# Performance work log

Hardware: AMD Instinct MI355X
Metric: run time of the kernel (lower is better)

Reference implementation:

```python
import jax, jax.numpy as jnp
import numpy as np

B, S, D_IN, H, L = 8, 4096, 256, 512, 2
EPS = 1e-5


def layer_norm(x, w, b):
    mu = x.mean(axis=-1, keepdims=True)
    var = ((x - mu) ** 2).mean(axis=-1, keepdims=True)
    return (x - mu) * jax.lax.rsqrt(var + EPS) * w + b


def rwkv_scan(k, v):
    # wkv_t = sigmoid(k_t)*v_t + alpha_{t-1};  alpha_t = sigmoid(k_t)*v_t + 0.9*alpha_{t-1}
    s = jax.nn.sigmoid(k) * v  # [B,S,H]
    def step(alpha, s_t):
        wkv_t = s_t + alpha
        return s_t + 0.9 * alpha, wkv_t
    _, wkv = jax.lax.scan(step, jnp.zeros_like(s[:, 0]), jnp.swapaxes(s, 0, 1))
    return jnp.swapaxes(wkv, 0, 1)


def setup_inputs() -> dict:
    key = jax.random.key(0)
    ks = jax.random.split(key, 16)
    sc = 1.0 / np.sqrt(H)
    return {
        "x": jax.random.normal(ks[0], (B, S, D_IN), jnp.float32),
        "W_in": jax.random.normal(ks[1], (H, D_IN), jnp.float32) / np.sqrt(D_IN),
        "b_in": jnp.zeros((H,), jnp.float32),
        "tm_k": jax.random.normal(ks[2], (L, H), jnp.float32),
        "tm_v": jax.random.normal(ks[3], (L, H), jnp.float32),
        "tm_r": jax.random.normal(ks[4], (L, H), jnp.float32),
        "Wk": jax.random.normal(ks[5], (L, H, H), jnp.float32) * sc,
        "Wv": jax.random.normal(ks[6], (L, H, H), jnp.float32) * sc,
        "Wr": jax.random.normal(ks[7], (L, H, H), jnp.float32) * sc,
        "Wo": jax.random.normal(ks[8], (L, H, H), jnp.float32) * sc,
        "ln1_w": jnp.ones((L, H), jnp.float32),
        "ln1_b": jnp.zeros((L, H), jnp.float32),
        "ln2_w": jnp.ones((L, H), jnp.float32),
        "ln2_b": jnp.zeros((L, H), jnp.float32),
    }


def reference(x, W_in, b_in, tm_k, tm_v, tm_r, Wk, Wv, Wr, Wo, ln1_w, ln1_b, ln2_w, ln2_b):
    h = jnp.einsum('bsd,hd->bsh', x, W_in) + b_in  # input projection
    for l in range(L):
        mean = h.mean(axis=1, keepdims=True)  # [B,1,H]
        xk = h * tm_k[l] + (1 - tm_k[l]) * mean
        xv = h * tm_v[l] + (1 - tm_v[l]) * mean
        xr = h * tm_r[l] + (1 - tm_r[l]) * mean
        k = jax.nn.relu(jnp.einsum('bsh,oh->bso', xk, Wk[l]))
        v = jax.nn.relu(jnp.einsum('bsh,oh->bso', xv, Wv[l]))
        r = jax.nn.sigmoid(jnp.einsum('bsh,oh->bso', xr, Wr[l]))
        wkv = rwkv_scan(k, v)
        out = jnp.einsum('bsh,oh->bso', r * wkv, Wo[l])
        out = layer_norm(h + out, ln1_w[l], ln1_b[l])
        ff = jax.nn.relu(layer_norm(out, ln2_w[l], ln2_b[l]))
        h = out + ff
    return h
```

## Files before the change

### kernel.cpp

```cpp
#include <hip/hip_runtime.h>
#include <hip/hip_bf16.h>
#include <cstdint>
#include <cstddef>

#define S_LEN 4096
#define HDIM  512
#define BDIM  8
#define DIN   256
#define NLAYER 2

using float4v = __attribute__((ext_vector_type(4))) float;
using short8  = __attribute__((ext_vector_type(8))) short;
using bf16x8  = __attribute__((ext_vector_type(8))) __bf16;

struct __align__(8) us4_t { unsigned short x, y, z, w; };

__device__ __forceinline__ unsigned short f2bf(float f) {
    return __builtin_bit_cast(unsigned short, (__bf16)f);
}
__device__ __forceinline__ float bf2f(unsigned short s) {
    union { unsigned u; float f; } v; v.u = ((unsigned)s) << 16;
    return v.f;
}
__device__ __forceinline__ float fast_rcp(float x) { return __builtin_amdgcn_rcpf(x); }
__device__ __forceinline__ float fast_rsq(float x) { return __builtin_amdgcn_rsqf(x); }

__device__ __forceinline__ float4v mfma_bf16(short8 a, short8 b, float4v c) {
    return __builtin_amdgcn_mfma_f32_16x16x32_bf16(
        __builtin_bit_cast(bf16x8, a), __builtin_bit_cast(bf16x8, b), c, 0, 0, 0);
}
__device__ __forceinline__ float wave_sum(float v) {
#pragma unroll
    for (int m = 1; m < 64; m <<= 1) v += __shfl_xor(v, m, 64);
    return v;
}
__device__ __forceinline__ void gload16(const void* g, void* l) {
    __builtin_amdgcn_global_load_lds(
        (const __attribute__((address_space(1))) unsigned int*)g,
        (__attribute__((address_space(3))) unsigned int*)l,
        16, 0, 0);
}

#define VMW_ASM(N) asm volatile("s_waitcnt vmcnt(" #N ")" ::: "memory")
template<int N> __device__ __forceinline__ void vmwait() {
    static_assert(N == 0 || N == 4 || N == 6 || N == 8 || N == 10,
                  "add a case for this N");
    if constexpr (N == 0) VMW_ASM(0);
    else if constexpr (N == 4) VMW_ASM(4);
    else if constexpr (N == 6) VMW_ASM(6);
    else if constexpr (N == 8) VMW_ASM(8);
    else if constexpr (N == 10) VMW_ASM(10);
}
#define LGKM0()    asm volatile("s_waitcnt lgkmcnt(0)" ::: "memory")
#define RBARRIER() asm volatile("s_barrier" ::: "memory")

__global__ void cvt_k(const float* __restrict__ in, unsigned short* __restrict__ out, int n4) {
    int i = blockIdx.x * blockDim.x + threadIdx.x;
    if (i >= n4) return;
    float4 v = ((const float4*)in)[i];
    us4_t o;
    o.x = f2bf(v.x); o.y = f2bf(v.y); o.z = f2bf(v.z); o.w = f2bf(v.w);
    ((us4_t*)out)[i] = o;
}

__global__ void cvtw_k(const float* __restrict__ Wk, const float* __restrict__ Wv,
                       const float* __restrict__ Wr,
                       const float* __restrict__ tmk, const float* __restrict__ tmv,
                       const float* __restrict__ tmr,
                       unsigned short* __restrict__ Wf)
{
    int i = blockIdx.x * blockDim.x + threadIdx.x;
    int e = i * 4;
    if (e >= NLAYER * 3 * HDIM * HDIM) return;
    const int HH = HDIM * HDIM;
    int l   = (e >= 3 * HH) ? 1 : 0;
    int rem = e - l * 3 * HH;
    int j   = rem >> 18;
    int ok  = rem & (HH - 1);
    int k   = ok & (HDIM - 1);
    const float* W = (j == 0) ? Wk : (j == 1) ? Wv : Wr;
    const float* t = (j == 0) ? tmk : (j == 1) ? tmv : tmr;
    float4 w = *(const float4*)(W + (size_t)l * HH + ok);
    const float* tp = t + l * HDIM + k;
    us4_t o;
    o.x = f2bf(w.x * tp[0]); o.y = f2bf(w.y * tp[1]);
    o.z = f2bf(w.z * tp[2]); o.w = f2bf(w.w * tp[3]);
    *(us4_t*)(Wf + e) = o;
}

__global__ void meanbias_k(const float* __restrict__ msum_l, float invS,
    const float* __restrict__ Wk, const float* __restrict__ Wv, const float* __restrict__ Wr,
    const float* __restrict__ tmk, const float* __restrict__ tmv, const float* __restrict__ tmr,
    float* __restrict__ mb)
{
    __shared__ float m2[HDIM];
    const int j = blockIdx.x, b = blockIdx.y, oc = blockIdx.z;
    const int tid = threadIdx.x, lane = tid & 63, wid = tid >> 6;
    const float* W = (j == 0) ? Wk : (j == 1) ? Wv : Wr;
    const float* t = (j == 0) ? tmk : (j == 1) ? tmv : tmr;
    for (int i = tid; i < HDIM; i += 256)
        m2[i] = msum_l[b * HDIM + i] * invS * (1.f - t[i]);
    __syncthreads();
    const int o0 = oc * 64 + wid * 16;
    for (int oo = 0; oo < 16; oo++) {
        int o = o0 + oo;
        const float* wr_ = W + (size_t)o * HDIM + lane * 8;
        float4 w0 = *(const float4*)wr_;
        float4 w1 = *(const float4*)(wr_ + 4);
        const float* mp = m2 + lane * 8;
        float s = w0.x * mp[0] + w0.y * mp[1] + w0.z * mp[2] + w0.w * mp[3]
                + w1.x * mp[4] + w1.y * mp[5] + w1.z * mp[6] + w1.w * mp[7];
        s = wave_sum(s);
        if (lane == 0) mb[((size_t)j * BDIM + b) * HDIM + o] = s;
    }
}

template<int TM, int BN, int NMAT, int EPI, int K, int NY>
__global__ __launch_bounds__(256, 2) void gemm2_k(
    const unsigned short* __restrict__ A,
    const unsigned short* __restrict__ B0,
    const unsigned short* __restrict__ B1,
    const unsigned short* __restrict__ B2,
    const float* __restrict__ mb,
    unsigned short* __restrict__ outB0,
    unsigned short* __restrict__ outB1,
    float* __restrict__ msum_out)
{
    constexpr int NT   = K / 64;
    static_assert(NT >= 2, "pipeline needs >=2 K-tiles");
    constexpr int ROWS = TM + NMAT * BN;
    constexpr int NC   = ROWS / 8;
    constexpr int NCW  = NC / 4;
    constexpr int MI   = TM / 32;
    constexpr int NI   = BN / 32;
    __shared__ __align__(16) unsigned short smem[2][ROWS * 64];

    const int tid = threadIdx.x, lane = tid & 63, wid = tid >> 6;
    const int wr = wid >> 1, wc = wid & 1;
    const int chunk = gridDim.x >> 3;
    const int logical = (blockIdx.x & 7) * chunk + (blockIdx.x >> 3);
    const int m0 = (logical / NY) * TM, n0 = (logical % NY) * BN;

    const int l8 = lane >> 3;
    const int soff = (((lane & 7) ^ l8) * 16);
    const char* gp[NCW];
#pragma unroll
    for (int i = 0; i < NCW; i++) {
        int c = wid * NCW + i;
        const unsigned short* base; int row;
        if (c < TM / 8) { base = A; row = m0 + c * 8 + l8; }
        else {
            int cb = c - TM / 8;
            int j  = cb / (BN / 8);
            int rl = (cb % (BN / 8)) * 8 + l8;
            base = (j == 0) ? B0 : ((j == 1) ? B1 : B2);
            row  = n0 + rl;
        }
        gp[i] = (const char*)base + (size_t)row * (K * 2) + soff;
    }

    float4v acc[NMAT][MI][NI];
#pragma unroll
    for (int j = 0; j < NMAT; j++)
#pragma unroll
        for (int mi = 0; mi < MI; mi++)
#pragma unroll
            for (int ni = 0; ni < NI; ni++)
                acc[j][mi][ni] = (float4v){0.f, 0.f, 0.f, 0.f};

    auto STAGE = [&](int buf) {
#pragma unroll
        for (int i = 0; i < NCW; i++) {
            gload16(gp[i], (char*)&smem[buf][0] + (unsigned)(wid * NCW + i) * 1024);
            gp[i] += 128;
        }
    };

    STAGE(0);
    STAGE(1);
    for (int t = 0; t < NT; t++) {
        if (t == NT - 1) vmwait<0>(); else vmwait<NCW>();
        RBARRIER();
        const int cur = t & 1;
        const unsigned short* As = &smem[cur][0];
        const unsigned short* Bs = &smem[cur][TM * 64];
#pragma unroll
        for (int kk = 0; kk < 2; kk++) {
            short8 a_[MI];
#pragma unroll
            for (int mi = 0; mi < MI; mi++) {
                int row = wr * (TM / 2) + mi * 16 + (lane & 15);
                int sl  = (kk * 4 + (lane >> 4)) ^ (row & 7);
                a_[mi] = *(const short8*)&As[row * 64 + sl * 8];
            }
#pragma unroll
            for (int ni = 0; ni < NI; ni++) {
                int rowb = wc * (BN / 2) + ni * 16 + (lane & 15);
                int slb  = (kk * 4 + (lane >> 4)) ^ (rowb & 7);
#pragma unroll
                for (int j = 0; j < NMAT; j++) {
                    short8 b_ = *(const short8*)&Bs[(j * BN + rowb) * 64 + slb * 8];
#pragma unroll
                    for (int mi = 0; mi < MI; mi++)
                        acc[j][mi][ni] = mfma_bf16(a_[mi], b_, acc[j][mi][ni]);
                }
            }
        }
        LGKM0();
        RBARRIER();
        if (t + 2 < NT) STAGE(cur);
    }

    const int bidx  = m0 >> 12;
    const int rbl   = wr * (TM / 2) + (lane >> 4) * 4;
    const int cbl   = wc * (BN / 2) + (lane & 15);

    if (EPI == 0) {
        constexpr int BNP = BN + 8;
        unsigned short* tile = &smem[0][0];
        float csum[NI];
#pragma unroll
        for (int ni = 0; ni < NI; ni++) csum[ni] = 0.f;
#pragma unroll
        for (int ni = 0; ni < NI; ni++) {
            float bb = mb[n0 + cbl + ni * 16];
#pragma unroll
            for (int mi = 0; mi < MI; mi++) {
#pragma unroll
                for (int r = 0; r < 4; r++) {
                    float val = acc[0][mi][ni][r] + bb;
                    tile[(rbl + mi * 16 + r) * BNP + cbl + ni * 16] = f2bf(val);
                    csum[ni] += val;
                }
            }
        }
        __syncthreads();
        constexpr int QR = BN / 8;
        for (int idx = tid; idx < TM * QR; idx += 256) {
            int row = idx / QR, q = idx % QR;
            int4 v = *(const int4*)&tile[row * BNP + q * 8];
            *(int4*)(outB0 + (size_t)(m0 + row) * HDIM + n0 + q * 8) = v;
        }
#pragma unroll
        for (int ni = 0; ni < NI; ni++) {
            float sc = csum[ni];
            sc += __shfl_xor(sc, 16, 64);
            sc += __shfl_xor(sc, 32, 64);
            if (lane < 16)
                atomicAdd(&msum_out[bidx * HDIM + n0 + wc * (BN / 2) + ni * 16 + lane], sc);
        }
    } else if (EPI == 1) {
        constexpr int BNP = BN + 8;
        unsigned short* tS = &smem[0][0];
        unsigned short* tR = &smem[0][0] + TM * BNP;
#pragma unroll
        for (int ni = 0; ni < NI; ni++) {
            int gcol = n0 + cbl + ni * 16;
            float mk = mb[(0 * BDIM + bidx) * HDIM + gcol];
            float mv = mb[(1 * BDIM + bidx) * HDIM + gcol];
            float mr = mb[(2 * BDIM + bidx) * HDIM + gcol];
#pragma unroll
            for (int mi = 0; mi < MI; mi++) {
#pragma unroll
                for (int r = 0; r < 4; r++) {
                    float kk_ = fmaxf(acc[0][mi][ni][r] + mk, 0.f);
                    float vv  = fmaxf(acc[1][mi][ni][r] + mv, 0.f);
                    float rr  = fast_rcp(1.f + __expf(-(acc[2][mi][ni][r] + mr)));
                    float sv  = vv * fast_rcp(1.f + __expf(-kk_));
                    int loc = (rbl + mi * 16 + r) * BNP + cbl + ni * 16;
                    tS[loc] = f2bf(sv);
                    tR[loc] = f2bf(rr);
                }
            }
        }
        __syncthreads();
        constexpr int QR = BN / 8;
        for (int idx = tid; idx < 2 * TM * QR; idx += 256) {
            int tn = idx / (TM * QR), rem = idx % (TM * QR);
            int row = rem / QR, q = rem % QR;
            int4 v = *(const int4*)&smem[0][tn * TM * BNP + row * BNP + q * 8];
            unsigned short* dst = tn ? outB1 : outB0;
            *(int4*)(dst + (size_t)(m0 + row) * HDIM + n0 + q * 8) = v;
        }
    } else {
        constexpr int BNP = BN + 8;
        unsigned short* tile = &smem[0][0];
#pragma unroll
        for (int ni = 0; ni < NI; ni++) {
#pragma unroll
            for (int mi = 0; mi < MI; mi++) {
#pragma unroll
                for (int r = 0; r < 4; r++)
                    tile[(rbl + mi * 16 + r) * BNP + cbl + ni * 16] = f2bf(acc[0][mi][ni][r]);
            }
        }
        __syncthreads();
        constexpr int QR = BN / 8;
        for (int idx = tid; idx < TM * QR; idx += 256) {
            int row = idx / QR, q = idx % QR;
            int4 v = *(const int4*)&tile[row * BNP + q * 8];
            *(int4*)(outB0 + (size_t)(m0 + row) * HDIM + n0 + q * 8) = v;
        }
    }
}

__global__ void scan_k(const unsigned short* __restrict__ s_bf,
                       const unsigned short* __restrict__ r_bf,
                       unsigned short* __restrict__ y_bf)
{
    const int C = 64, W = 64;
    const int b  = blockIdx.z;
    const int p  = blockIdx.x;
    const int c  = ((p & 7) << 3) | (p >> 3);
    const int t0 = c * C;
    const int h2 = threadIdx.x * 2;
    const size_t rowbase = (size_t)b * S_LEN;

    float a0 = 0.f, a1 = 0.f;
    int tstart = t0 - W; if (tstart < 0) tstart = 0;
#pragma unroll 4
    for (int t = tstart; t < t0; t++) {
        unsigned u = *(const unsigned*)(s_bf + (rowbase + t) * HDIM + h2);
        a0 = bf2f((unsigned short)(u & 0xffff)) + 0.9f * a0;
        a1 = bf2f((unsigned short)(u >> 16))    + 0.9f * a1;
    }
#pragma unroll 4
    for (int t = t0; t < t0 + C; t++) {
        size_t off = (rowbase + t) * HDIM + h2;
        unsigned u  = *(const unsigned*)(s_bf + off);
        unsigned ur = *(const unsigned*)(r_bf + off);
        float s0 = bf2f((unsigned short)(u & 0xffff));
        float s1 = bf2f((unsigned short)(u >> 16));
        float w0 = s0 + a0, w1v = s1 + a1;
        a0 = s0 + 0.9f * a0;
        a1 = s1 + 0.9f * a1;
        float r0 = bf2f((unsigned short)(ur & 0xffff));
        float r1 = bf2f((unsigned short)(ur >> 16));
        unsigned outp = (unsigned)f2bf(r0 * w0) | ((unsigned)f2bf(r1 * w1v) << 16);
        *(unsigned*)(y_bf + off) = outp;
    }
}

__global__ __launch_bounds__(256) void lnfuse_k(
    const unsigned short* __restrict__ Hb, const unsigned short* __restrict__ O,
    const float* __restrict__ w1, const float* __restrict__ b1,
    const float* __restrict__ w2, const float* __restrict__ b2,
    float* __restrict__ dstF, unsigned short* __restrict__ dst_bf,
    float* __restrict__ msum_next)
{
    __shared__ float red[HDIM];
    const int b    = blockIdx.y;
    const int tid  = threadIdx.x;
    const int wid  = tid >> 6, lane = tid & 63;
    const int wglob = blockIdx.x * 4 + wid;
    const int c0   = lane * 8;

    float w1v[8], b1v[8], w2v[8], b2v[8];
#pragma unroll
    for (int j = 0; j < 8; j++) {
        w1v[j] = w1[c0 + j]; b1v[j] = b1[c0 + j];
        w2v[j] = w2[c0 + j]; b2v[j] = b2[c0 + j];
    }
    float macc[8] = {0.f, 0.f, 0.f, 0.f, 0.f, 0.f, 0.f, 0.f};

    for (int s = wglob; s < S_LEN; s += 512) {
        size_t ro = ((size_t)b * S_LEN + s) * HDIM + c0;
        int4 hv4 = *(const int4*)(Hb + ro);
        int4 ov4 = *(const int4*)(O + ro);
        const unsigned short* hu = (const unsigned short*)&hv4;
        const unsigned short* ou = (const unsigned short*)&ov4;
        float x[8];
#pragma unroll
        for (int j = 0; j < 8; j++) x[j] = bf2f(hu[j]) + bf2f(ou[j]);
        float sm = 0.f;
#pragma unroll
        for (int j = 0; j < 8; j++) sm += x[j];
        float mu = wave_sum(sm) * (1.f / HDIM);
        float sq = 0.f;
#pragma unroll
        for (int j = 0; j < 8; j++) { float d = x[j] - mu; sq += d * d; }
        float rs = fast_rsq(wave_sum(sq) * (1.f / HDIM) + 1e-5f);
        float out[8];
#pragma unroll
        for (int j = 0; j < 8; j++) out[j] = (x[j] - mu) * rs * w1v[j] + b1v[j];
        float sm2 = 0.f;
#pragma unroll
        for (int j = 0; j < 8; j++) sm2 += out[j];
        float mu2 = wave_sum(sm2) * (1.f / HDIM);
        float sq2 = 0.f;
#pragma unroll
        for (int j = 0; j < 8; j++) { float d = out[j] - mu2; sq2 += d * d; }
        float rs2 = fast_rsq(wave_sum(sq2) * (1.f / HDIM) + 1e-5f);
        float hn[8];
#pragma unroll
        for (int j = 0; j < 8; j++) {
            float ff = fmaxf(0.f, (out[j] - mu2) * rs2 * w2v[j] + b2v[j]);
            hn[j] = out[j] + ff;
            macc[j] += hn[j];
        }
        if (dstF) {
            float4 o1 = {hn[0], hn[1], hn[2], hn[3]};
            float4 o2 = {hn[4], hn[5], hn[6], hn[7]};
            *(float4*)(dstF + ro) = o1;
            *(float4*)(dstF + ro + 4) = o2;
        }
        if (dst_bf) {
            unsigned q[4];
#pragma unroll
            for (int j = 0; j < 4; j++)
                q[j] = (unsigned)f2bf(hn[2 * j]) | ((unsigned)f2bf(hn[2 * j + 1]) << 16);
            *(int4*)(dst_bf + ro) = *(int4*)q;
        }
    }

    if (msum_next) {
        for (int i = tid; i < HDIM; i += 256) red[i] = 0.f;
        __syncthreads();
#pragma unroll
        for (int j = 0; j < 8; j++) atomicAdd(&red[c0 + j], macc[j]);
        __syncthreads();
        for (int i = tid; i < HDIM; i += 256)
            atomicAdd(&msum_next[b * HDIM + i], red[i]);
    }
}

extern "C" void kernel_launch(void* const* d_in, const int* in_sizes, int n_in,
                              void* d_out, int out_size, void* d_ws, size_t ws_size,
                              hipStream_t stream)
{
    const float* x   = (const float*)d_in[0];
    const float* Win = (const float*)d_in[1];
    const float* bin = (const float*)d_in[2];
    const float* tmk = (const float*)d_in[3];
    const float* tmv = (const float*)d_in[4];
    const float* tmr = (const float*)d_in[5];
    const float* Wk  = (const float*)d_in[6];
    const float* Wv  = (const float*)d_in[7];
    const float* Wr  = (const float*)d_in[8];
    const float* Wo  = (const float*)d_in[9];
    const float* l1w = (const float*)d_in[10];
    const float* l1b = (const float*)d_in[11];
    const float* l2w = (const float*)d_in[12];
    const float* l2b = (const float*)d_in[13];

    char* ws = (char*)d_ws;
    size_t off = 0;
    auto alloc = [&](size_t bytes) -> char* {
        char* p = ws + off;
        off += (bytes + 255) & ~(size_t)255;
        return p;
    };
    const size_t NTOK = (size_t)BDIM * S_LEN;
    const size_t HH = (size_t)HDIM * HDIM;
    unsigned short* region0 = (unsigned short*)alloc(NTOK * HDIM * 2);
    unsigned short* x_bf   = region0;
    unsigned short* y_bf   = region0;
    unsigned short* Win_bf = (unsigned short*)alloc((size_t)HDIM * DIN * 2);
    unsigned short* Wo_bf  = (unsigned short*)alloc(NLAYER * HH * 2);
    unsigned short* Wf     = (unsigned short*)alloc(NLAYER * 3 * HH * 2);
    unsigned short* h_bf   = (unsigned short*)alloc(NTOK * HDIM * 2);
    unsigned short* h2_bf  = (unsigned short*)alloc(NTOK * HDIM * 2);
    unsigned short* s_bf   = (unsigned short*)alloc(NTOK * HDIM * 2);
    unsigned short* r_bf   = (unsigned short*)alloc(NTOK * HDIM * 2);
    unsigned short* o_bf   = (unsigned short*)alloc(NTOK * HDIM * 2);
    float*          msum   = (float*)alloc(2 * BDIM * HDIM * 4);
    float*          mbuf   = (float*)alloc(3 * BDIM * HDIM * 4);

    hipMemsetAsync(msum, 0, 2 * BDIM * HDIM * 4, stream);

    auto cvt = [&](const float* src, unsigned short* dst, size_t n) {
        int n4 = (int)(n / 4);
        cvt_k<<<(n4 + 255) / 256, 256, 0, stream>>>(src, dst, n4);
    };
    cvt(x,   x_bf,   NTOK * DIN);
    cvt(Win, Win_bf, (size_t)HDIM * DIN);
    cvt(Wo,  Wo_bf,  NLAYER * HH);
    {
        int n4 = NLAYER * 3 * HH / 4;
        cvtw_k<<<(n4 + 255) / 256, 256, 0, stream>>>(Wk, Wv, Wr, tmk, tmv, tmr, Wf);
    }

    const float invS = 1.f / S_LEN;

    gemm2_k<128, 64, 1, 0, DIN, 8><<<2048, 256, 0, stream>>>(
        x_bf, Win_bf, nullptr, nullptr, bin, h_bf, nullptr, msum);

    for (int l = 0; l < NLAYER; l++) {
        const unsigned short* hl = (l == 0) ? h_bf : h2_bf;
        meanbias_k<<<dim3(3, BDIM, 8), 256, 0, stream>>>(
            msum + (size_t)l * BDIM * HDIM, invS,
            Wk + (size_t)l * HH, Wv + (size_t)l * HH, Wr + (size_t)l * HH,
            tmk + l * HDIM, tmv + l * HDIM, tmr + l * HDIM, mbuf);
        gemm2_k<128, 64, 3, 1, HDIM, 8><<<2048, 256, 0, stream>>>(
            hl,
            Wf + ((size_t)l * 3 + 0) * HH, Wf + ((size_t)l * 3 + 1) * HH,
            Wf + ((size_t)l * 3 + 2) * HH,
            mbuf, s_bf, r_bf, nullptr);
        scan_k<<<dim3(S_LEN / 64, 1, BDIM), 256, 0, stream>>>(s_bf, r_bf, y_bf);
        gemm2_k<128, 64, 1, 3, HDIM, 8><<<2048, 256, 0, stream>>>(
            y_bf, Wo_bf + (size_t)l * HH, nullptr, nullptr,
            nullptr, o_bf, nullptr, nullptr);
        lnfuse_k<<<dim3(128, BDIM), 256, 0, stream>>>(
            hl, o_bf, l1w + l * HDIM, l1b + l * HDIM, l2w + l * HDIM, l2b + l * HDIM,
            (l == 0) ? nullptr : (float*)d_out,
            (l == 0) ? h2_bf : nullptr,
            (l == 0) ? (msum + BDIM * HDIM) : nullptr);
    }
}
```

Baseline: 339.9 us.

## Add single-buffer GEMM variant for higher occupancy; widen tiles for input/output GEMMs

Adds a DBUF template flag to the GEMM. The fused k/v/r GEMM switches to a single-buffered LDS loop with launch bounds of 4 blocks per CU, trading intra-block load/compute overlap for more resident blocks. The input and output projection GEMMs move to 128x128 tiles with half the blocks while keeping double buffering. The scan kernel also drops its block-index swizzle and uses a linear chunk mapping.

```diff
diff --git a/kernel.cpp b/kernel.cpp
--- a/kernel.cpp
+++ b/kernel.cpp
@@ -115,8 +115,8 @@
     }
 }
 
-template<int TM, int BN, int NMAT, int EPI, int K, int NY>
-__global__ __launch_bounds__(256, 2) void gemm2_k(
+template<int TM, int BN, int NMAT, int EPI, int K, int NY, int DBUF>
+__global__ __launch_bounds__(256, DBUF ? 2 : 4) void gemm2_k(
     const unsigned short* __restrict__ A,
     const unsigned short* __restrict__ B0,
     const unsigned short* __restrict__ B1,
@@ -133,7 +133,10 @@
     constexpr int NCW  = NC / 4;
     constexpr int MI   = TM / 32;
     constexpr int NI   = BN / 32;
-    __shared__ __align__(16) unsigned short smem[2][ROWS * 64];
+    constexpr int NBUF = DBUF ? 2 : 1;
+    __shared__ __align__(16) unsigned short smem[NBUF][ROWS * 64];
+    static_assert((EPI == 1 ? 2 : 1) * TM * (BN + 8) <= NBUF * ROWS * 64,
+                  "epilogue overflow");
 
     const int tid = threadIdx.x, lane = tid & 63, wid = tid >> 6;
     const int wr = wid >> 1, wc = wid & 1;
@@ -175,15 +178,7 @@
             gp[i] += 128;
         }
     };
-
-    STAGE(0);
-    STAGE(1);
-    for (int t = 0; t < NT; t++) {
-        if (t == NT - 1) vmwait<0>(); else vmwait<NCW>();
-        RBARRIER();
-        const int cur = t & 1;
-        const unsigned short* As = &smem[cur][0];
-        const unsigned short* Bs = &smem[cur][TM * 64];
+    auto COMPUTE = [&](const unsigned short* As, const unsigned short* Bs) {
 #pragma unroll
         for (int kk = 0; kk < 2; kk++) {
             short8 a_[MI];
@@ -206,16 +201,36 @@
                 }
             }
         }
-        LGKM0();
-        RBARRIER();
-        if (t + 2 < NT) STAGE(cur);
+    };
+
+    if constexpr (DBUF) {
+        STAGE(0);
+        STAGE(1);
+        for (int t = 0; t < NT; t++) {
+            if (t == NT - 1) vmwait<0>(); else vmwait<NCW>();
+            RBARRIER();
+            const int cur = t & 1;
+            COMPUTE(&smem[cur][0], &smem[cur][TM * 64]);
+            LGKM0();
+            RBARRIER();
+            if (t + 2 < NT) STAGE(cur);
+        }
+    } else {
+        for (int t = 0; t < NT; t++) {
+            STAGE(0);
+            vmwait<0>();
+            RBARRIER();
+            COMPUTE(&smem[0][0], &smem[0][TM * 64]);
+            LGKM0();
+            RBARRIER();
+        }
     }
 
     const int bidx  = m0 >> 12;
     const int rbl   = wr * (TM / 2) + (lane >> 4) * 4;
     const int cbl   = wc * (BN / 2) + (lane & 15);
 
-    if (EPI == 0) {
+    if constexpr (EPI == 0) {
         constexpr int BNP = BN + 8;
         unsigned short* tile = &smem[0][0];
         float csum[NI];
@@ -249,7 +264,7 @@
             if (lane < 16)
                 atomicAdd(&msum_out[bidx * HDIM + n0 + wc * (BN / 2) + ni * 16 + lane], sc);
         }
-    } else if (EPI == 1) {
+    } else if constexpr (EPI == 1) {
         constexpr int BNP = BN + 8;
         unsigned short* tS = &smem[0][0];
         unsigned short* tR = &smem[0][0] + TM * BNP;
@@ -264,8 +279,8 @@
 #pragma unroll
                 for (int r = 0; r < 4; r++) {
                     float kk_ = fmaxf(acc[0][mi][ni][r] + mk, 0.f);
-                    float vv  = fmaxf(acc[1][mi][ni][r] + mv, 0.f);
-                    float rr  = fast_rcp(1.f + __expf(-(acc[2][mi][ni][r] + mr)));
+                    float vv  = fmaxf(acc[NMAT > 1 ? 1 : 0][mi][ni][r] + mv, 0.f);
+                    float rr  = fast_rcp(1.f + __expf(-(acc[NMAT > 2 ? 2 : 0][mi][ni][r] + mr)));
                     float sv  = vv * fast_rcp(1.f + __expf(-kk_));
                     int loc = (rbl + mi * 16 + r) * BNP + cbl + ni * 16;
                     tS[loc] = f2bf(sv);
@@ -310,9 +325,7 @@
 {
     const int C = 64, W = 64;
     const int b  = blockIdx.z;
-    const int p  = blockIdx.x;
-    const int c  = ((p & 7) << 3) | (p >> 3);
-    const int t0 = c * C;
+    const int t0 = blockIdx.x * C;
     const int h2 = threadIdx.x * 2;
     const size_t rowbase = (size_t)b * S_LEN;
 
@@ -482,7 +495,7 @@
 
     const float invS = 1.f / S_LEN;
 
-    gemm2_k<128, 64, 1, 0, DIN, 8><<<2048, 256, 0, stream>>>(
+    gemm2_k<128, 128, 1, 0, DIN, 4, 1><<<1024, 256, 0, stream>>>(
         x_bf, Win_bf, nullptr, nullptr, bin, h_bf, nullptr, msum);
 
     for (int l = 0; l < NLAYER; l++) {
@@ -491,13 +504,13 @@
             msum + (size_t)l * BDIM * HDIM, invS,
             Wk + (size_t)l * HH, Wv + (size_t)l * HH, Wr + (size_t)l * HH,
             tmk + l * HDIM, tmv + l * HDIM, tmr + l * HDIM, mbuf);
-        gemm2_k<128, 64, 3, 1, HDIM, 8><<<2048, 256, 0, stream>>>(
+        gemm2_k<128, 64, 3, 1, HDIM, 8, 0><<<2048, 256, 0, stream>>>(
             hl,
             Wf + ((size_t)l * 3 + 0) * HH, Wf + ((size_t)l * 3 + 1) * HH,
             Wf + ((size_t)l * 3 + 2) * HH,
             mbuf, s_bf, r_bf, nullptr);
         scan_k<<<dim3(S_LEN / 64, 1, BDIM), 256, 0, stream>>>(s_bf, r_bf, y_bf);
-        gemm2_k<128, 64, 1, 3, HDIM, 8><<<2048, 256, 0, stream>>>(
+        gemm2_k<128, 128, 1, 3, HDIM, 4, 1><<<1024, 256, 0, stream>>>(
             y_bf, Wo_bf + (size_t)l * HH, nullptr, nullptr,
             nullptr, o_bf, nullptr, nullptr);
         lnfuse_k<<<dim3(128, BDIM), 256, 0, stream>>>(
```

Measured after the change: 353.2 us. 1.04x slower.
